# Performance work log

Measured on AMD Instinct MI355X. Metric: run time of the kernel, lower is better.

## Reference

```python
import jax, jax.numpy as jnp
import numpy as np

B, S, H = 1024, 512, 768
NUM_CLASSES = 3


def setup_inputs() -> dict:
    key = jax.random.key(0)
    k1, k2, k3, k4 = jax.random.split(key, 4)
    embeddings = jax.random.normal(k1, (B, S, H), dtype=jnp.float32)
    # labels 0..4; 2/3/4 mark pronoun, entity A, entity B tokens
    mentions = jax.random.randint(k2, (B, S), 0, 5, dtype=jnp.int64)
    W1 = jax.random.normal(k3, (3 * H, 512), dtype=jnp.float32) * 0.02
    b1 = jnp.zeros((512,), dtype=jnp.float32)
    W2 = jax.random.normal(k4, (512, NUM_CLASSES), dtype=jnp.float32) * 0.02
    b2 = jnp.zeros((NUM_CLASSES,), dtype=jnp.float32)
    return {"embeddings": embeddings, "mentions": mentions,
            "W1": W1, "b1": b1, "W2": W2, "b2": b2}


def _masked_mean(embeddings, mentions, label):
    # embeddings: [B,S,H], mentions: [B,S] -> [B,H]
    mask = (mentions == label).astype(embeddings.dtype)  # [B,S]
    s = jnp.einsum('bsh,bs->bh', embeddings, mask)
    c = jnp.sum(mask, axis=1, keepdims=True)             # [B,1]
    return s / c


def reference(embeddings, mentions, W1, b1, W2, b2):
    # Dropout is identity in eval mode. Vectorized replacement of the
    # python loop + growing torch.cat: three segment-mean pools, concat,
    # then 2-layer MLP classifier.
    pronouns = _masked_mean(embeddings, mentions, 2)
    entities_a = _masked_mean(embeddings, mentions, 3)
    entities_b = _masked_mean(embeddings, mentions, 4)
    o = jnp.concatenate([pronouns, entities_a, entities_b], axis=-1)  # [B,3H]
    h = jax.nn.relu(o @ W1 + b1)
    return h @ W2 + b2
```

## Files before the change

kernel.cpp:

```cpp
#include <hip/hip_runtime.h>
#include <hip/hip_bf16.h>

#define B_SZ 1024
#define S_SZ 512
#define H_SZ 768
#define K3H  2304
#define HID  512
#define NC   3

typedef __attribute__((ext_vector_type(8)))  __bf16        bf16x8;
typedef __attribute__((ext_vector_type(16))) float         f32x16;
typedef __attribute__((ext_vector_type(8)))  unsigned short ushort8x;

__device__ __forceinline__ unsigned short f2bf(float f) {
    unsigned u = __builtin_bit_cast(unsigned, f);
    unsigned r = (u + 0x7fffu + ((u >> 16) & 1u)) >> 16;
    return (unsigned short)r;
}

__global__ __launch_bounds__(192) void pool_kernel(
        const float* __restrict__ emb,
        const int*   __restrict__ men,
        unsigned short* __restrict__ o)
{
    const int b = blockIdx.x;
    const int t = threadIdx.x;

    __shared__ unsigned short sel[S_SZ];
    __shared__ int nsel_sh;
    __shared__ int cnt[3];

    if (t < 64) {
        int basep = 0;
        int c0 = 0, c1 = 0, c2 = 0;
        #pragma unroll
        for (int ch = 0; ch < 8; ++ch) {
            int s = ch * 64 + t;
            int m = men[(size_t)b * S_SZ + s];
            bool pick = (m >= 2);
            unsigned long long mk = __ballot(pick);
            int pos = basep + __popcll(mk & ((1ull << t) - 1ull));
            if (pick) sel[pos] = (unsigned short)(s | ((m - 2) << 12));
            basep += __popcll(mk);
            c0 += (m == 2);
            c1 += (m == 3);
            c2 += (m == 4);
        }
        #pragma unroll
        for (int off = 32; off > 0; off >>= 1) {
            c0 += __shfl_down(c0, off);
            c1 += __shfl_down(c1, off);
            c2 += __shfl_down(c2, off);
        }
        if (t == 0) { nsel_sh = basep; cnt[0] = c0; cnt[1] = c1; cnt[2] = c2; }
    }
    __syncthreads();

    const int ns = nsel_sh;
    float4 a0 = {0.f,0.f,0.f,0.f}, a1 = {0.f,0.f,0.f,0.f}, a2 = {0.f,0.f,0.f,0.f};
    const float4* base =
        reinterpret_cast<const float4*>(emb + (size_t)b * S_SZ * H_SZ);

    #define ACCUM(E, V) do {                                             \
        int tg_ = (E) >> 12;                                             \
        if (tg_ == 0)      { a0.x+=V.x; a0.y+=V.y; a0.z+=V.z; a0.w+=V.w; } \
        else if (tg_ == 1) { a1.x+=V.x; a1.y+=V.y; a1.z+=V.z; a1.w+=V.w; } \
        else               { a2.x+=V.x; a2.y+=V.y; a2.z+=V.z; a2.w+=V.w; } \
    } while (0)

    int i = 0;
    for (; i + 4 <= ns; i += 4) {
        int e0 = sel[i], e1 = sel[i+1], e2 = sel[i+2], e3 = sel[i+3];
        float4 v0 = base[(e0 & 0x1ff) * 192 + t];
        float4 v1 = base[(e1 & 0x1ff) * 192 + t];
        float4 v2 = base[(e2 & 0x1ff) * 192 + t];
        float4 v3 = base[(e3 & 0x1ff) * 192 + t];
        ACCUM(e0, v0); ACCUM(e1, v1); ACCUM(e2, v2); ACCUM(e3, v3);
    }
    for (; i < ns; ++i) {
        int e = sel[i];
        float4 v = base[(e & 0x1ff) * 192 + t];
        ACCUM(e, v);
    }
    #undef ACCUM

    const float r0 = 1.f / (float)cnt[0];
    const float r1 = 1.f / (float)cnt[1];
    const float r2 = 1.f / (float)cnt[2];

    unsigned short* op = o + (size_t)b * K3H;
    ushort4 w0 = { f2bf(a0.x*r0), f2bf(a0.y*r0), f2bf(a0.z*r0), f2bf(a0.w*r0) };
    ushort4 w1 = { f2bf(a1.x*r1), f2bf(a1.y*r1), f2bf(a1.z*r1), f2bf(a1.w*r1) };
    ushort4 w2 = { f2bf(a2.x*r2), f2bf(a2.y*r2), f2bf(a2.z*r2), f2bf(a2.w*r2) };
    *reinterpret_cast<ushort4*>(op + 0 * H_SZ + t * 4) = w0;
    *reinterpret_cast<ushort4*>(op + 1 * H_SZ + t * 4) = w1;
    *reinterpret_cast<ushort4*>(op + 2 * H_SZ + t * 4) = w2;
}

__global__ __launch_bounds__(256) void transpose_kernel(
        const float* __restrict__ W1, unsigned short* __restrict__ Bt)
{
    __shared__ unsigned short tile[32][33];
    const int kb = blockIdx.x * 32, nb = blockIdx.y * 32;
    const int c = threadIdx.x & 31, r0 = threadIdx.x >> 5;
    #pragma unroll
    for (int i = 0; i < 4; ++i) {
        int r = r0 + i * 8;
        tile[r][c] = f2bf(W1[(size_t)(kb + r) * HID + nb + c]);
    }
    __syncthreads();
    #pragma unroll
    for (int i = 0; i < 4; ++i) {
        int r = r0 + i * 8;
        Bt[(size_t)(nb + r) * K3H + kb + c] = tile[c][r];
    }
}

__global__ __launch_bounds__(256) void mlp1_kernel(
        const unsigned short* __restrict__ A,
        const unsigned short* __restrict__ Bt,
        const float* __restrict__ bias,
        float*       __restrict__ C)
{
    __shared__ unsigned short lds[2][2][64 * 64];

    const int t  = threadIdx.x;
    const int m0 = blockIdx.y * 64;
    const int n0 = blockIdx.x * 64;
    const int w  = t >> 6, l = t & 63;
    const int wr = w >> 1, wc = w & 1;
    const int lr = l & 31;
    const int hi = l >> 5;
    const int sw = lr & 7;

    const int s_row0 = t >> 3;
    const int s_row1 = 32 + (t >> 3);
    const int s_slot = t & 7;

    const unsigned short* a_p0 = A  + (size_t)(m0 + s_row0) * K3H + s_slot * 8;
    const unsigned short* a_p1 = A  + (size_t)(m0 + s_row1) * K3H + s_slot * 8;
    const unsigned short* b_p0 = Bt + (size_t)(n0 + s_row0) * K3H + s_slot * 8;
    const unsigned short* b_p1 = Bt + (size_t)(n0 + s_row1) * K3H + s_slot * 8;

    const int w_idx0 = s_row0 * 64 + ((s_slot ^ (s_row0 & 7)) * 8);
    const int w_idx1 = s_row1 * 64 + ((s_slot ^ (s_row1 & 7)) * 8);

    f32x16 acc = {0.f,0.f,0.f,0.f,0.f,0.f,0.f,0.f,
                  0.f,0.f,0.f,0.f,0.f,0.f,0.f,0.f};

    ushort8x ra0 = *(const ushort8x*)(a_p0);
    ushort8x ra1 = *(const ushort8x*)(a_p1);
    ushort8x rb0 = *(const ushort8x*)(b_p0);
    ushort8x rb1 = *(const ushort8x*)(b_p1);
    *(ushort8x*)&lds[0][0][w_idx0] = ra0;
    *(ushort8x*)&lds[0][0][w_idx1] = ra1;
    *(ushort8x*)&lds[0][1][w_idx0] = rb0;
    *(ushort8x*)&lds[0][1][w_idx1] = rb1;
    __syncthreads();

    const int NT = K3H / 64;
    int cur = 0;
    const int a_frag_row = (wr * 32 + lr) * 64;
    const int b_frag_row = (wc * 32 + lr) * 64;

    for (int step = 0; step < NT; ++step) {
        if (step + 1 < NT) {
            const size_t koff = (size_t)(step + 1) * 64;
            ra0 = *(const ushort8x*)(a_p0 + koff);
            ra1 = *(const ushort8x*)(a_p1 + koff);
            rb0 = *(const ushort8x*)(b_p0 + koff);
            rb1 = *(const ushort8x*)(b_p1 + koff);
        }

        const unsigned short* As = lds[cur][0];
        const unsigned short* Bs = lds[cur][1];
        #pragma unroll
        for (int kk = 0; kk < 64; kk += 16) {
            const int ks = (kk >> 3) + hi;
            bf16x8 af = *(const bf16x8*)&As[a_frag_row + ((ks ^ sw) * 8)];
            bf16x8 bf = *(const bf16x8*)&Bs[b_frag_row + ((ks ^ sw) * 8)];
            acc = __builtin_amdgcn_mfma_f32_32x32x16_bf16(af, bf, acc, 0, 0, 0);
        }
        __syncthreads();

        if (step + 1 < NT) {
            const int nb = cur ^ 1;
            *(ushort8x*)&lds[nb][0][w_idx0] = ra0;
            *(ushort8x*)&lds[nb][0][w_idx1] = ra1;
            *(ushort8x*)&lds[nb][1][w_idx0] = rb0;
            *(ushort8x*)&lds[nb][1][w_idx1] = rb1;
            __syncthreads();
            cur = nb;
        }
    }

    const int col = n0 + wc * 32 + lr;
    const float bv = bias[col];
    #pragma unroll
    for (int r = 0; r < 16; ++r) {
        int row = (r & 3) + 8 * (r >> 2) + 4 * hi;
        float v = acc[r] + bv;
        C[(size_t)(m0 + wr * 32 + row) * HID + col] = fmaxf(v, 0.f);
    }
}

__global__ __launch_bounds__(64) void mlp2_kernel(
        const float* __restrict__ h,
        const float* __restrict__ W2,
        const float* __restrict__ b2,
        float*       __restrict__ out)
{
    const int b = blockIdx.x;
    const int l = threadIdx.x;
    float a0 = 0.f, a1 = 0.f, a2 = 0.f;
    for (int k = l; k < HID; k += 64) {
        float hv = h[(size_t)b * HID + k];
        a0 += hv * W2[k * 3 + 0];
        a1 += hv * W2[k * 3 + 1];
        a2 += hv * W2[k * 3 + 2];
    }
    #pragma unroll
    for (int off = 32; off > 0; off >>= 1) {
        a0 += __shfl_down(a0, off);
        a1 += __shfl_down(a1, off);
        a2 += __shfl_down(a2, off);
    }
    if (l == 0) {
        out[b * 3 + 0] = a0 + b2[0];
        out[b * 3 + 1] = a1 + b2[1];
        out[b * 3 + 2] = a2 + b2[2];
    }
}

extern "C" void kernel_launch(void* const* d_in, const int* in_sizes, int n_in,
                              void* d_out, int out_size, void* d_ws, size_t ws_size,
                              hipStream_t stream) {
    const float* emb = (const float*)d_in[0];
    const int*   men = (const int*)  d_in[1];
    const float* W1  = (const float*)d_in[2];
    const float* b1  = (const float*)d_in[3];
    const float* W2  = (const float*)d_in[4];
    const float* b2  = (const float*)d_in[5];
    float* out = (float*)d_out;

    unsigned short* o_bf = (unsigned short*)d_ws;
    unsigned short* w1t  = o_bf + (size_t)B_SZ * K3H;
    float*          h    = (float*)(w1t + (size_t)HID * K3H);

    transpose_kernel<<<dim3(K3H / 32, HID / 32), 256, 0, stream>>>(W1, w1t);
    pool_kernel<<<B_SZ, 192, 0, stream>>>(emb, men, o_bf);
    mlp1_kernel<<<dim3(HID / 64, B_SZ / 64), 256, 0, stream>>>(o_bf, w1t, b1, h);
    mlp2_kernel<<<B_SZ, 64, 0, stream>>>(h, W2, b2, out);
}
```

Before: 215.0 us.

## Fuse W1 transpose into pool kernel and split-K the first MLP GEMM

The W1 bf16 transpose now runs as extra blocks (64x64 tiles) appended to the pooling kernel's grid, which removes one launch and lets the transpose overlap with pooling. The first GEMM is split into two K halves (grid z=2), doubling the block count from 128 to 256 to fill more CUs. Each half writes raw fp32 partials. The second-layer kernel sums the two partials, adds bias and applies ReLU, and now packs 4 rows per block. The trade-off is an extra fp32 partial buffer and its read traffic.

```diff
diff --git a/kernel.cpp b/kernel.cpp
--- a/kernel.cpp
+++ b/kernel.cpp
@@ -7,6 +7,7 @@
 #define K3H  2304
 #define HID  512
 #define NC   3
+#define KSPLIT_HALF 1152
 
 typedef __attribute__((ext_vector_type(8)))  __bf16        bf16x8;
 typedef __attribute__((ext_vector_type(16))) float         f32x16;
@@ -18,14 +19,33 @@
     return (unsigned short)r;
 }
 
-__global__ __launch_bounds__(192) void pool_kernel(
+__global__ __launch_bounds__(192) void pool_tr_kernel(
         const float* __restrict__ emb,
         const int*   __restrict__ men,
-        unsigned short* __restrict__ o)
+        const float* __restrict__ W1,
+        unsigned short* __restrict__ o,
+        unsigned short* __restrict__ Bt)
 {
+    const int t = threadIdx.x;
+
+    if (blockIdx.x >= B_SZ) {
+        __shared__ unsigned short tile[64][65];
+        const int bt = blockIdx.x - B_SZ;
+        const int kb = (bt >> 3) * 64;
+        const int nb = (bt & 7) * 64;
+        for (int i = t; i < 4096; i += 192) {
+            int r = i >> 6, c = i & 63;
+            tile[r][c] = f2bf(W1[(size_t)(kb + r) * HID + nb + c]);
+        }
+        __syncthreads();
+        for (int i = t; i < 4096; i += 192) {
+            int rr = i >> 6, cc = i & 63;
+            Bt[(size_t)(nb + rr) * K3H + kb + cc] = tile[cc][rr];
+        }
+        return;
+    }
+
     const int b = blockIdx.x;
-    const int t = threadIdx.x;
-
     __shared__ unsigned short sel[S_SZ];
     __shared__ int nsel_sh;
     __shared__ int cnt[3];
@@ -97,36 +117,19 @@
     *reinterpret_cast<ushort4*>(op + 2 * H_SZ + t * 4) = w2;
 }
 
-__global__ __launch_bounds__(256) void transpose_kernel(
-        const float* __restrict__ W1, unsigned short* __restrict__ Bt)
-{
-    __shared__ unsigned short tile[32][33];
-    const int kb = blockIdx.x * 32, nb = blockIdx.y * 32;
-    const int c = threadIdx.x & 31, r0 = threadIdx.x >> 5;
-    #pragma unroll
-    for (int i = 0; i < 4; ++i) {
-        int r = r0 + i * 8;
-        tile[r][c] = f2bf(W1[(size_t)(kb + r) * HID + nb + c]);
-    }
-    __syncthreads();
-    #pragma unroll
-    for (int i = 0; i < 4; ++i) {
-        int r = r0 + i * 8;
-        Bt[(size_t)(nb + r) * K3H + kb + c] = tile[c][r];
-    }
-}
-
 __global__ __launch_bounds__(256) void mlp1_kernel(
         const unsigned short* __restrict__ A,
         const unsigned short* __restrict__ Bt,
-        const float* __restrict__ bias,
-        float*       __restrict__ C)
+        float*       __restrict__ hp)
 {
     __shared__ unsigned short lds[2][2][64 * 64];
 
     const int t  = threadIdx.x;
     const int m0 = blockIdx.y * 64;
     const int n0 = blockIdx.x * 64;
+    const int kz = blockIdx.z;
+    const int kbase = kz * KSPLIT_HALF;
+
     const int w  = t >> 6, l = t & 63;
     const int wr = w >> 1, wc = w & 1;
     const int lr = l & 31;
@@ -137,10 +140,10 @@
     const int s_row1 = 32 + (t >> 3);
     const int s_slot = t & 7;
 
-    const unsigned short* a_p0 = A  + (size_t)(m0 + s_row0) * K3H + s_slot * 8;
-    const unsigned short* a_p1 = A  + (size_t)(m0 + s_row1) * K3H + s_slot * 8;
-    const unsigned short* b_p0 = Bt + (size_t)(n0 + s_row0) * K3H + s_slot * 8;
-    const unsigned short* b_p1 = Bt + (size_t)(n0 + s_row1) * K3H + s_slot * 8;
+    const unsigned short* a_p0 = A  + (size_t)(m0 + s_row0) * K3H + kbase + s_slot * 8;
+    const unsigned short* a_p1 = A  + (size_t)(m0 + s_row1) * K3H + kbase + s_slot * 8;
+    const unsigned short* b_p0 = Bt + (size_t)(n0 + s_row0) * K3H + kbase + s_slot * 8;
+    const unsigned short* b_p1 = Bt + (size_t)(n0 + s_row1) * K3H + kbase + s_slot * 8;
 
     const int w_idx0 = s_row0 * 64 + ((s_slot ^ (s_row0 & 7)) * 8);
     const int w_idx1 = s_row1 * 64 + ((s_slot ^ (s_row1 & 7)) * 8);
@@ -158,7 +161,7 @@
     *(ushort8x*)&lds[0][1][w_idx1] = rb1;
     __syncthreads();
 
-    const int NT = K3H / 64;
+    const int NT = KSPLIT_HALF / 64;
     int cur = 0;
     const int a_frag_row = (wr * 32 + lr) * 64;
     const int b_frag_row = (wc * 32 + lr) * 64;
@@ -194,27 +197,34 @@
         }
     }
 
+    float* out = hp + (size_t)kz * B_SZ * HID;
     const int col = n0 + wc * 32 + lr;
-    const float bv = bias[col];
     #pragma unroll
     for (int r = 0; r < 16; ++r) {
         int row = (r & 3) + 8 * (r >> 2) + 4 * hi;
-        float v = acc[r] + bv;
-        C[(size_t)(m0 + wr * 32 + row) * HID + col] = fmaxf(v, 0.f);
-    }
-}
-
-__global__ __launch_bounds__(64) void mlp2_kernel(
-        const float* __restrict__ h,
+        out[(size_t)(m0 + wr * 32 + row) * HID + col] = acc[r];
+    }
+}
+
+__global__ __launch_bounds__(256) void mlp2_kernel(
+        const float* __restrict__ hp,
+        const float* __restrict__ b1,
         const float* __restrict__ W2,
         const float* __restrict__ b2,
         float*       __restrict__ out)
 {
-    const int b = blockIdx.x;
-    const int l = threadIdx.x;
+    const int w = threadIdx.x >> 6;
+    const int l = threadIdx.x & 63;
+    const int b = blockIdx.x * 4 + w;
+
+    const float* h0 = hp + (size_t)b * HID;
+    const float* h1 = hp + (size_t)B_SZ * HID + (size_t)b * HID;
+
     float a0 = 0.f, a1 = 0.f, a2 = 0.f;
-    for (int k = l; k < HID; k += 64) {
-        float hv = h[(size_t)b * HID + k];
+    #pragma unroll
+    for (int kk = 0; kk < HID; kk += 64) {
+        int k = kk + l;
+        float hv = fmaxf(h0[k] + h1[k] + b1[k], 0.f);
         a0 += hv * W2[k * 3 + 0];
         a1 += hv * W2[k * 3 + 1];
         a2 += hv * W2[k * 3 + 2];
@@ -245,10 +255,9 @@
 
     unsigned short* o_bf = (unsigned short*)d_ws;
     unsigned short* w1t  = o_bf + (size_t)B_SZ * K3H;
-    float*          h    = (float*)(w1t + (size_t)HID * K3H);
-
-    transpose_kernel<<<dim3(K3H / 32, HID / 32), 256, 0, stream>>>(W1, w1t);
-    pool_kernel<<<B_SZ, 192, 0, stream>>>(emb, men, o_bf);
-    mlp1_kernel<<<dim3(HID / 64, B_SZ / 64), 256, 0, stream>>>(o_bf, w1t, b1, h);
-    mlp2_kernel<<<B_SZ, 64, 0, stream>>>(h, W2, b2, out);
-}
+    float*          hp   = (float*)(w1t + (size_t)HID * K3H);
+
+    pool_tr_kernel<<<B_SZ + 288, 192, 0, stream>>>(emb, men, W1, o_bf, w1t);
+    mlp1_kernel<<<dim3(8, 16, 2), 256, 0, stream>>>(o_bf, w1t, hp);
+    mlp2_kernel<<<256, 256, 0, stream>>>(hp, b1, W2, b2, out);
+}
```

Result: faster. 197.8 us (-8.0%).
